# Optimization experiments

Hardware: AMD Instinct MI355X
Metric: run time of the kernel (lower is better)

Reference implementation:

```python
import jax, jax.numpy as jnp
import numpy as np
from jax import lax

NX = NY = NZ = 64
H = 1.0
BIG = 1000.0  # 'infinity' init value used by the torch module
N_EVENT = 4096


def _seed_u0(v, x, y, z):
    """Faithful port of Eikonal3D.set_u0: seed travel time at the 8 grid nodes
    surrounding the source (x,y,z in physical coords), rest = BIG."""
    ix0 = jnp.clip(jnp.floor(x / H), 0, NX - 2).astype(jnp.int32)
    iy0 = jnp.clip(jnp.floor(y / H), 0, NY - 2).astype(jnp.int32)
    iz0 = jnp.clip(jnp.floor(z / H), 0, NZ - 2).astype(jnp.int32)
    xs = jnp.clip(x, 0.0, (NX - 1) * H) / H
    ys = jnp.clip(y, 0.0, (NY - 1) * H) / H
    zs = jnp.clip(z, 0.0, (NZ - 1) * H) / H
    u0 = jnp.full((NX, NY, NZ), BIG, dtype=v.dtype)
    for dx in (0, 1):
        for dy in (0, 1):
            for dz in (0, 1):
                ii, jj, kk = ix0 + dx, iy0 + dy, iz0 + dz
                dist = jnp.sqrt((xs - ii) ** 2 + (ys - jj) ** 2 + (zs - kk) ** 2)
                u0 = u0.at[ii, jj, kk].set(dist * H / v[ii, jj, kk])
    return u0


def _godunov_update(u, fh):
    """One Jacobi pass of the Godunov upwind local eikonal solver |grad u| = f."""
    up = jnp.pad(u, 1, constant_values=BIG * 10.0)
    ax = jnp.minimum(up[:-2, 1:-1, 1:-1], up[2:, 1:-1, 1:-1])
    ay = jnp.minimum(up[1:-1, :-2, 1:-1], up[1:-1, 2:, 1:-1])
    az = jnp.minimum(up[1:-1, 1:-1, :-2], up[1:-1, 1:-1, 2:])
    a = jnp.sort(jnp.stack([ax, ay, az], axis=0), axis=0)
    a1, a2, a3 = a[0], a[1], a[2]
    # 1-direction candidate
    x1 = a1 + fh
    # 2-direction candidate
    d2 = 2.0 * fh * fh - (a1 - a2) ** 2
    x2 = 0.5 * (a1 + a2 + jnp.sqrt(jnp.maximum(d2, 0.0)))
    # 3-direction candidate
    s = a1 + a2 + a3
    q = a1 * a1 + a2 * a2 + a3 * a3
    d3 = s * s - 3.0 * (q - fh * fh)
    x3 = (s + jnp.sqrt(jnp.maximum(d3, 0.0))) / 3.0
    unew = jnp.where(x1 <= a2, x1, jnp.where(x2 <= a3, x2, x3))
    return jnp.minimum(u, unew)


def _interp(tbl, x, y, z):
    """Faithful port of Eikonal3D.interp (trilinear, with the module's exact
    clamp semantics: indices from unclamped coords, weights from clamped)."""
    ix0 = jnp.clip(jnp.floor(x / H), 0, NX - 2).astype(jnp.int32)
    iy0 = jnp.clip(jnp.floor(y / H), 0, NY - 2).astype(jnp.int32)
    iz0 = jnp.clip(jnp.floor(z / H), 0, NZ - 2).astype(jnp.int32)
    ix1, iy1, iz1 = ix0 + 1, iy0 + 1, iz0 + 1
    xs = jnp.clip(x, 0.0, (NX - 1) * H) / H
    ys = jnp.clip(y, 0.0, (NY - 1) * H) / H
    zs = jnp.clip(z, 0.0, (NZ - 1) * H) / H
    wx1, wx0 = ix1 - xs, xs - ix0
    wy1, wy0 = iy1 - ys, ys - iy0
    wz1, wz0 = iz1 - zs, zs - iz0
    t = (tbl[ix0, iy0, iz0] * wx1 * wy1 * wz1 + tbl[ix1, iy0, iz0] * wx0 * wy1 * wz1
         + tbl[ix0, iy1, iz0] * wx1 * wy0 * wz1 + tbl[ix1, iy1, iz0] * wx0 * wy0 * wz1
         + tbl[ix0, iy0, iz1] * wx1 * wy1 * wz0 + tbl[ix1, iy0, iz1] * wx0 * wy1 * wz0
         + tbl[ix0, iy1, iz1] * wx1 * wy0 * wz0 + tbl[ix1, iy1, iz1] * wx0 * wy0 * wz0)
    return t


def setup_inputs() -> dict:
    key = jax.random.key(0)
    k1, k2, k3, k4, k5 = jax.random.split(key, 5)
    vp = 5.0 + 2.0 * jax.random.uniform(k1, (NX, NY, NZ), dtype=jnp.float32)
    station_loc = jax.random.uniform(k2, (3,), dtype=jnp.float32) * (NX - 1) * H
    event_loc = jax.random.uniform(k3, (N_EVENT, 3), dtype=jnp.float32) * (NX - 1) * H
    event_time = jax.random.normal(k4, (N_EVENT,), dtype=jnp.float32)
    phase_time = jax.random.normal(k5, (N_EVENT,), dtype=jnp.float32) + 10.0
    return {"vp": vp, "station_loc": station_loc, "event_loc": event_loc,
            "event_time": event_time, "phase_time": phase_time, "n_iter": 128}


def reference(vp, station_loc, event_loc, event_time, phase_time, n_iter):
    fh = (1.0 / vp) * H  # slowness * grid spacing
    u0 = _seed_u0(vp, station_loc[0], station_loc[1], station_loc[2])
    u, _ = lax.scan(lambda u, _: (_godunov_update(u, fh), None), u0, None, length=n_iter)
    tt = _interp(u, event_loc[:, 0], event_loc[:, 1], event_loc[:, 2])
    at = event_time + tt  # predicted arrival time per pick
    loss = jnp.mean((at - phase_time) ** 2)
    return at, loss
```

## Files before the change

### kernel.cpp

```cpp
#include <hip/hip_runtime.h>
#include <hip/hip_bf16.h>


#define NXg 64
#define NYg 64
#define NZg 64
#define NPTS (NXg * NYg * NZg)
#define BIGV 1000.0f
#define PADV 10000.0f
#define NEV 4096

__global__ __launch_bounds__(256) void eik_init(const float* __restrict__ vp,
                                                const float* __restrict__ st,
                                                float* __restrict__ u,
                                                float* __restrict__ fh) {
    int idx = blockIdx.x * blockDim.x + threadIdx.x;
    if (idx >= NPTS) return;
    float v = vp[idx];
    fh[idx] = 1.0f / v;

    int z = idx & 63;
    int y = (idx >> 6) & 63;
    int x = idx >> 12;

    float sx = st[0], sy = st[1], sz = st[2];
    int ix0 = min(max((int)floorf(sx), 0), NXg - 2);
    int iy0 = min(max((int)floorf(sy), 0), NYg - 2);
    int iz0 = min(max((int)floorf(sz), 0), NZg - 2);
    float xs = fminf(fmaxf(sx, 0.0f), (float)(NXg - 1));
    float ys = fminf(fmaxf(sy, 0.0f), (float)(NYg - 1));
    float zs = fminf(fmaxf(sz, 0.0f), (float)(NZg - 1));

    float val = BIGV;
    if (x >= ix0 && x <= ix0 + 1 && y >= iy0 && y <= iy0 + 1 &&
        z >= iz0 && z <= iz0 + 1) {
        float dx = xs - (float)x;
        float dy = ys - (float)y;
        float dz = zs - (float)z;
        float dist = sqrtf(dx * dx + dy * dy + dz * dz);
        val = dist / v;
    }
    u[idx] = val;
}

__global__ __launch_bounds__(256) void eik_godunov(const float* __restrict__ u,
                                                   float* __restrict__ un,
                                                   const float* __restrict__ fh) {
    int idx = blockIdx.x * blockDim.x + threadIdx.x;
    if (idx >= NPTS) return;
    int z = idx & 63;
    int y = (idx >> 6) & 63;
    int x = idx >> 12;

    float uc = u[idx];
    float xm = (x > 0)       ? u[idx - 4096] : PADV;
    float xp = (x < NXg - 1) ? u[idx + 4096] : PADV;
    float ym = (y > 0)       ? u[idx - 64]   : PADV;
    float yp = (y < NYg - 1) ? u[idx + 64]   : PADV;
    float zm = (z > 0)       ? u[idx - 1]    : PADV;
    float zp = (z < NZg - 1) ? u[idx + 1]    : PADV;

    float ax = fminf(xm, xp);
    float ay = fminf(ym, yp);
    float az = fminf(zm, zp);

    float lo = fminf(ax, ay), hi = fmaxf(ax, ay);
    float a1 = fminf(lo, az);
    float a3 = fmaxf(hi, az);
    float a2 = fminf(fmaxf(lo, az), hi);

    float f = fh[idx];

    float x1 = a1 + f;
    float d12 = a1 - a2;
    float d2 = 2.0f * f * f - d12 * d12;
    float x2 = 0.5f * (a1 + a2 + sqrtf(fmaxf(d2, 0.0f)));
    float s = a1 + a2 + a3;
    float q = a1 * a1 + a2 * a2 + a3 * a3;
    float d3 = s * s - 3.0f * (q - f * f);
    float x3 = (s + sqrtf(fmaxf(d3, 0.0f))) * (1.0f / 3.0f);

    float unew = (x1 <= a2) ? x1 : ((x2 <= a3) ? x2 : x3);
    un[idx] = fminf(uc, unew);
}

__global__ __launch_bounds__(1024) void eik_finalize(const float* __restrict__ u,
                                                     const float* __restrict__ evloc,
                                                     const float* __restrict__ evtime,
                                                     const float* __restrict__ phtime,
                                                     float* __restrict__ out) {
    __shared__ float red[16];
    int t = threadIdx.x;
    float acc = 0.0f;
    for (int i = t; i < NEV; i += 1024) {
        float x = evloc[3 * i + 0];
        float y = evloc[3 * i + 1];
        float z = evloc[3 * i + 2];
        int ix0 = min(max((int)floorf(x), 0), NXg - 2);
        int iy0 = min(max((int)floorf(y), 0), NYg - 2);
        int iz0 = min(max((int)floorf(z), 0), NZg - 2);
        float xs = fminf(fmaxf(x, 0.0f), (float)(NXg - 1));
        float ys = fminf(fmaxf(y, 0.0f), (float)(NYg - 1));
        float zs = fminf(fmaxf(z, 0.0f), (float)(NZg - 1));
        float wx0 = xs - (float)ix0, wx1 = (float)(ix0 + 1) - xs;
        float wy0 = ys - (float)iy0, wy1 = (float)(iy0 + 1) - ys;
        float wz0 = zs - (float)iz0, wz1 = (float)(iz0 + 1) - zs;
        int base = ix0 * 4096 + iy0 * 64 + iz0;
        float c000 = u[base];
        float c100 = u[base + 4096];
        float c010 = u[base + 64];
        float c110 = u[base + 4096 + 64];
        float c001 = u[base + 1];
        float c101 = u[base + 4096 + 1];
        float c011 = u[base + 64 + 1];
        float c111 = u[base + 4096 + 64 + 1];
        float tt = c000 * wx1 * wy1 * wz1 + c100 * wx0 * wy1 * wz1
                 + c010 * wx1 * wy0 * wz1 + c110 * wx0 * wy0 * wz1
                 + c001 * wx1 * wy1 * wz0 + c101 * wx0 * wy1 * wz0
                 + c011 * wx1 * wy0 * wz0 + c111 * wx0 * wy0 * wz0;
        float at = evtime[i] + tt;
        out[i] = at;
        float d = at - phtime[i];
        acc += d * d;
    }
    #pragma unroll
    for (int off = 32; off > 0; off >>= 1) acc += __shfl_down(acc, off);
    if ((t & 63) == 0) red[t >> 6] = acc;
    __syncthreads();
    if (t < 16) {
        float v = red[t];
        #pragma unroll
        for (int off = 8; off > 0; off >>= 1) v += __shfl_down(v, off);
        if (t == 0) out[NEV] = v * (1.0f / (float)NEV);
    }
}

extern "C" void kernel_launch(void* const* d_in, const int* in_sizes, int n_in,
                              void* d_out, int out_size, void* d_ws, size_t ws_size,
                              hipStream_t stream) {
    const float* vp     = (const float*)d_in[0];
    const float* stloc  = (const float*)d_in[1];
    const float* evloc  = (const float*)d_in[2];
    const float* evtime = (const float*)d_in[3];
    const float* phtime = (const float*)d_in[4];
    float* out = (float*)d_out;

    float* w   = (float*)d_ws;
    float* u0  = w;
    float* u1  = w + NPTS;
    float* fh  = w + 2 * NPTS;

    const int NITER = 128;

    eik_init<<<NPTS / 256, 256, 0, stream>>>(vp, stloc, u0, fh);

    float* cur = u0;
    float* nxt = u1;
    for (int it = 0; it < NITER; ++it) {
        eik_godunov<<<NPTS / 256, 256, 0, stream>>>(cur, nxt, fh);
        float* tmp = cur; cur = nxt; nxt = tmp;
    }

    eik_finalize<<<1, 1024, 0, stream>>>(cur, evloc, evtime, phtime, out);
}
```

Before: 355.5 us.

## Fuse four Jacobi sweeps per launch with halo tiles and skip converged blocks

Replaces the 128 per-sweep launches with 32 launches. Each launch loads an 8^3 tile plus a 4-cell halo into LDS and runs four Godunov sweeps on shrinking regions, which removes most launches and global memory traffic. It also keeps per-block change flags. A block whose 27 neighbours did not change in the previous group just copies its tile forward. This adds redundant halo compute, higher LDS use, and flag bookkeeping that must stay exact with respect to the Jacobi semantics.

```diff
diff --git a/kernel.cpp b/kernel.cpp
--- a/kernel.cpp
+++ b/kernel.cpp
@@ -3,74 +3,24 @@
 
 
 #define NXg 64
-#define NYg 64
-#define NZg 64
-#define NPTS (NXg * NYg * NZg)
+#define NPTS (64 * 64 * 64)
 #define BIGV 1000.0f
 #define PADV 10000.0f
 #define NEV 4096
 
-__global__ __launch_bounds__(256) void eik_init(const float* __restrict__ vp,
-                                                const float* __restrict__ st,
-                                                float* __restrict__ u,
-                                                float* __restrict__ fh) {
-    int idx = blockIdx.x * blockDim.x + threadIdx.x;
-    if (idx >= NPTS) return;
-    float v = vp[idx];
-    fh[idx] = 1.0f / v;
-
-    int z = idx & 63;
-    int y = (idx >> 6) & 63;
-    int x = idx >> 12;
-
-    float sx = st[0], sy = st[1], sz = st[2];
-    int ix0 = min(max((int)floorf(sx), 0), NXg - 2);
-    int iy0 = min(max((int)floorf(sy), 0), NYg - 2);
-    int iz0 = min(max((int)floorf(sz), 0), NZg - 2);
-    float xs = fminf(fmaxf(sx, 0.0f), (float)(NXg - 1));
-    float ys = fminf(fmaxf(sy, 0.0f), (float)(NYg - 1));
-    float zs = fminf(fmaxf(sz, 0.0f), (float)(NZg - 1));
-
-    float val = BIGV;
-    if (x >= ix0 && x <= ix0 + 1 && y >= iy0 && y <= iy0 + 1 &&
-        z >= iz0 && z <= iz0 + 1) {
-        float dx = xs - (float)x;
-        float dy = ys - (float)y;
-        float dz = zs - (float)z;
-        float dist = sqrtf(dx * dx + dy * dy + dz * dz);
-        val = dist / v;
-    }
-    u[idx] = val;
-}
-
-__global__ __launch_bounds__(256) void eik_godunov(const float* __restrict__ u,
-                                                   float* __restrict__ un,
-                                                   const float* __restrict__ fh) {
-    int idx = blockIdx.x * blockDim.x + threadIdx.x;
-    if (idx >= NPTS) return;
-    int z = idx & 63;
-    int y = (idx >> 6) & 63;
-    int x = idx >> 12;
-
-    float uc = u[idx];
-    float xm = (x > 0)       ? u[idx - 4096] : PADV;
-    float xp = (x < NXg - 1) ? u[idx + 4096] : PADV;
-    float ym = (y > 0)       ? u[idx - 64]   : PADV;
-    float yp = (y < NYg - 1) ? u[idx + 64]   : PADV;
-    float zm = (z > 0)       ? u[idx - 1]    : PADV;
-    float zp = (z < NZg - 1) ? u[idx + 1]    : PADV;
-
-    float ax = fminf(xm, xp);
-    float ay = fminf(ym, yp);
-    float az = fminf(zm, zp);
-
+#define TB 8
+#define HALO 4
+#define RB 16
+#define ZS 20
+#define NBLK 512
+#define NGROUPS 32
+
+__device__ __forceinline__ float godunov_cell(float uc, float ax, float ay,
+                                              float az, float f) {
     float lo = fminf(ax, ay), hi = fmaxf(ax, ay);
     float a1 = fminf(lo, az);
     float a3 = fmaxf(hi, az);
     float a2 = fminf(fmaxf(lo, az), hi);
-
-    float f = fh[idx];
-
     float x1 = a1 + f;
     float d12 = a1 - a2;
     float d2 = 2.0f * f * f - d12 * d12;
@@ -79,9 +29,178 @@
     float q = a1 * a1 + a2 * a2 + a3 * a3;
     float d3 = s * s - 3.0f * (q - f * f);
     float x3 = (s + sqrtf(fmaxf(d3, 0.0f))) * (1.0f / 3.0f);
-
     float unew = (x1 <= a2) ? x1 : ((x2 <= a3) ? x2 : x3);
-    un[idx] = fminf(uc, unew);
+    return fminf(uc, unew);
+}
+
+__global__ __launch_bounds__(256) void eik_init(const float* __restrict__ vp,
+                                                const float* __restrict__ st,
+                                                float* __restrict__ u,
+                                                float* __restrict__ fh,
+                                                int* __restrict__ flags0) {
+    int idx = blockIdx.x * blockDim.x + threadIdx.x;
+    if (idx >= NPTS) return;
+    float v = vp[idx];
+    fh[idx] = 1.0f / v;
+
+    if (idx < NBLK) flags0[idx] = 1;
+
+    int z = idx & 63;
+    int y = (idx >> 6) & 63;
+    int x = idx >> 12;
+
+    float sx = st[0], sy = st[1], sz = st[2];
+    int ix0 = min(max((int)floorf(sx), 0), 62);
+    int iy0 = min(max((int)floorf(sy), 0), 62);
+    int iz0 = min(max((int)floorf(sz), 0), 62);
+    float xs = fminf(fmaxf(sx, 0.0f), 63.0f);
+    float ys = fminf(fmaxf(sy, 0.0f), 63.0f);
+    float zs = fminf(fmaxf(sz, 0.0f), 63.0f);
+
+    float val = BIGV;
+    if (x >= ix0 && x <= ix0 + 1 && y >= iy0 && y <= iy0 + 1 &&
+        z >= iz0 && z <= iz0 + 1) {
+        float dx = xs - (float)x;
+        float dy = ys - (float)y;
+        float dz = zs - (float)z;
+        val = sqrtf(dx * dx + dy * dy + dz * dz) / v;
+    }
+    u[idx] = val;
+}
+
+__global__ __launch_bounds__(256, 3) void eik_group(
+    const float* __restrict__ uCur, float* __restrict__ uNext,
+    const float* __restrict__ fh,
+    const int* __restrict__ chPrev, int* __restrict__ chNext) {
+    __shared__ float A[RB * RB * ZS];
+    __shared__ float B[RB * RB * ZS];
+    __shared__ float stash[TB * TB * TB];
+    __shared__ int s_any;
+
+    const int b = blockIdx.x;
+    const int BX = b >> 6, BY = (b >> 3) & 7, BZ = b & 7;
+    const int ox = BX * TB - HALO, oy = BY * TB - HALO, oz = BZ * TB - HALO;
+    const int tid = threadIdx.x;
+    const int tbase = ((BX * TB) * 64 + BY * TB) * 64 + BZ * TB;
+
+    if (tid == 0) s_any = 0;
+    __syncthreads();
+    if (tid < 27) {
+        int dx = tid / 9 - 1, dy = (tid / 3) % 3 - 1, dz = tid % 3 - 1;
+        int nx = BX + dx, ny = BY + dy, nz = BZ + dz;
+        if (nx >= 0 && nx < 8 && ny >= 0 && ny < 8 && nz >= 0 && nz < 8) {
+            if (chPrev[(nx << 6) | (ny << 3) | nz]) atomicOr(&s_any, 1);
+        }
+    }
+    __syncthreads();
+
+    if (!s_any) {
+        for (int u = tid; u < TB * TB * 2; u += 256) {
+            int c = u & 1, r = u >> 1;
+            int lx = r >> 3, ly = r & 7;
+            int goff = tbase + (lx * 64 + ly) * 64 + 4 * c;
+            *(float4*)&uNext[goff] = *(const float4*)&uCur[goff];
+        }
+        if (tid == 0) chNext[b] = 0;
+        return;
+    }
+
+    for (int u = tid; u < RB * RB * 4; u += 256) {
+        int c = u & 3, r = u >> 2;
+        int lx = r >> 4, ly = r & 15;
+        int gx = ox + lx, gy = oy + ly, gz0 = oz + 4 * c;
+        int loff = (lx * RB + ly) * ZS + 4 * c;
+        float4 v;
+        bool xyok = (gx >= 0) & (gx < 64) & (gy >= 0) & (gy < 64);
+        if (xyok && gz0 >= 0 && gz0 + 3 < 64) {
+            v = *(const float4*)&uCur[(gx * 64 + gy) * 64 + gz0];
+        } else {
+            int gb = (gx * 64 + gy) * 64;
+            v.x = (xyok && gz0 + 0 >= 0 && gz0 + 0 < 64) ? uCur[gb + gz0 + 0] : PADV;
+            v.y = (xyok && gz0 + 1 >= 0 && gz0 + 1 < 64) ? uCur[gb + gz0 + 1] : PADV;
+            v.z = (xyok && gz0 + 2 >= 0 && gz0 + 2 < 64) ? uCur[gb + gz0 + 2] : PADV;
+            v.w = (xyok && gz0 + 3 >= 0 && gz0 + 3 < 64) ? uCur[gb + gz0 + 3] : PADV;
+        }
+        *(float4*)&A[loff] = v;
+        *(float4*)&B[loff] = v;
+    }
+    __syncthreads();
+
+    for (int u = tid; u < TB * TB * 2; u += 256) {
+        int c = u & 1, r = u >> 1;
+        int lx = r >> 3, ly = r & 7;
+        int loff = ((lx + 4) * RB + (ly + 4)) * ZS + 4 + 4 * c;
+        *(float4*)&stash[(lx * 8 + ly) * 8 + 4 * c] = *(const float4*)&A[loff];
+    }
+
+    #pragma unroll
+    for (int it = 0; it < HALO; ++it) {
+        __syncthreads();
+        const float* src = (it & 1) ? B : A;
+        float* dst = (it & 1) ? A : B;
+        const int s0 = it + 1, s1 = 14 - it;
+        const int S = s1 - s0 + 1;
+        const int units = S * S * 4;
+        const int lzlo = max(s0, -oz);
+        const int lzhi = min(s1, 63 - oz);
+        for (int u = tid; u < units; u += 256) {
+            int c = u & 3, r = u >> 2;
+            int ly = s0 + (r % S), lx = s0 + (r / S);
+            int zb = 4 * c;
+            int rowoff = (lx * RB + ly) * ZS;
+            float4 cc = *(const float4*)&src[rowoff + zb];
+            float zmm = src[rowoff + zb - 1];
+            float zpp = src[rowoff + zb + 4];
+            float4 xm = *(const float4*)&src[rowoff - RB * ZS + zb];
+            float4 xp = *(const float4*)&src[rowoff + RB * ZS + zb];
+            float4 ym = *(const float4*)&src[rowoff - ZS + zb];
+            float4 yp = *(const float4*)&src[rowoff + ZS + zb];
+
+            int gx = ox + lx, gy = oy + ly, gz0 = oz + zb;
+            int cgx = min(max(gx, 0), 63), cgy = min(max(gy, 0), 63);
+            int cgz = min(max(gz0, 0), 60);
+            float4 f4 = *(const float4*)&fh[(cgx * 64 + cgy) * 64 + cgz];
+
+            float o0 = godunov_cell(cc.x, fminf(xm.x, xp.x), fminf(ym.x, yp.x),
+                                    fminf(zmm, cc.y), f4.x);
+            float o1 = godunov_cell(cc.y, fminf(xm.y, xp.y), fminf(ym.y, yp.y),
+                                    fminf(cc.x, cc.z), f4.y);
+            float o2 = godunov_cell(cc.z, fminf(xm.z, xp.z), fminf(ym.z, yp.z),
+                                    fminf(cc.y, cc.w), f4.z);
+            float o3 = godunov_cell(cc.w, fminf(xm.w, xp.w), fminf(ym.w, yp.w),
+                                    fminf(cc.z, zpp), f4.w);
+
+            bool xyin = (gx >= 0) & (gx < 64) & (gy >= 0) & (gy < 64);
+            int jlo = max(lzlo - zb, 0), jhi = min(lzhi - zb, 3);
+            if (xyin & (jlo == 0) & (jhi == 3)) {
+                *(float4*)&dst[rowoff + zb] = make_float4(o0, o1, o2, o3);
+            } else if (xyin) {
+                if (jlo <= 0 && 0 <= jhi) dst[rowoff + zb + 0] = o0;
+                if (jlo <= 1 && 1 <= jhi) dst[rowoff + zb + 1] = o1;
+                if (jlo <= 2 && 2 <= jhi) dst[rowoff + zb + 2] = o2;
+                if (jlo <= 3 && 3 <= jhi) dst[rowoff + zb + 3] = o3;
+            }
+        }
+    }
+    __syncthreads();
+
+    if (tid == 0) s_any = 0;
+    __syncthreads();
+    int changed = 0;
+    for (int u = tid; u < TB * TB * 2; u += 256) {
+        int c = u & 1, r = u >> 1;
+        int lx = r >> 3, ly = r & 7;
+        int loff = ((lx + 4) * RB + (ly + 4)) * ZS + 4 + 4 * c;
+        float4 v = *(const float4*)&A[loff];
+        float4 sv = *(const float4*)&stash[(lx * 8 + ly) * 8 + 4 * c];
+        int goff = tbase + (lx * 64 + ly) * 64 + 4 * c;
+        *(float4*)&uNext[goff] = v;
+        if (v.x != sv.x || v.y != sv.y || v.z != sv.z || v.w != sv.w) changed = 1;
+    }
+    int wch = __any(changed);
+    if ((tid & 63) == 0 && wch) atomicOr(&s_any, 1);
+    __syncthreads();
+    if (tid == 0) chNext[b] = s_any;
 }
 
 __global__ __launch_bounds__(1024) void eik_finalize(const float* __restrict__ u,
@@ -96,12 +215,12 @@
         float x = evloc[3 * i + 0];
         float y = evloc[3 * i + 1];
         float z = evloc[3 * i + 2];
-        int ix0 = min(max((int)floorf(x), 0), NXg - 2);
-        int iy0 = min(max((int)floorf(y), 0), NYg - 2);
-        int iz0 = min(max((int)floorf(z), 0), NZg - 2);
-        float xs = fminf(fmaxf(x, 0.0f), (float)(NXg - 1));
-        float ys = fminf(fmaxf(y, 0.0f), (float)(NYg - 1));
-        float zs = fminf(fmaxf(z, 0.0f), (float)(NZg - 1));
+        int ix0 = min(max((int)floorf(x), 0), 62);
+        int iy0 = min(max((int)floorf(y), 0), 62);
+        int iz0 = min(max((int)floorf(z), 0), 62);
+        float xs = fminf(fmaxf(x, 0.0f), 63.0f);
+        float ys = fminf(fmaxf(y, 0.0f), 63.0f);
+        float zs = fminf(fmaxf(z, 0.0f), 63.0f);
         float wx0 = xs - (float)ix0, wx1 = (float)(ix0 + 1) - xs;
         float wy0 = ys - (float)iy0, wy1 = (float)(iy0 + 1) - ys;
         float wz0 = zs - (float)iz0, wz1 = (float)(iz0 + 1) - zs;
@@ -145,21 +264,22 @@
     const float* phtime = (const float*)d_in[4];
     float* out = (float*)d_out;
 
-    float* w   = (float*)d_ws;
-    float* u0  = w;
-    float* u1  = w + NPTS;
-    float* fh  = w + 2 * NPTS;
-
-    const int NITER = 128;
-
-    eik_init<<<NPTS / 256, 256, 0, stream>>>(vp, stloc, u0, fh);
-
-    float* cur = u0;
-    float* nxt = u1;
-    for (int it = 0; it < NITER; ++it) {
-        eik_godunov<<<NPTS / 256, 256, 0, stream>>>(cur, nxt, fh);
-        float* tmp = cur; cur = nxt; nxt = tmp;
-    }
-
-    eik_finalize<<<1, 1024, 0, stream>>>(cur, evloc, evtime, phtime, out);
-}
+    float* w  = (float*)d_ws;
+    float* uA = w;
+    float* uB = w + NPTS;
+    float* fh = w + 2 * NPTS;
+    int* flA  = (int*)(w + 3 * NPTS);
+    int* flB  = flA + NBLK;
+
+    eik_init<<<NPTS / 256, 256, 0, stream>>>(vp, stloc, uA, fh, flA);
+
+    for (int g = 0; g < NGROUPS; ++g) {
+        const float* s = (g & 1) ? uB : uA;
+        float*       d = (g & 1) ? uA : uB;
+        const int*  fp = (g & 1) ? flB : flA;
+        int*        fn = (g & 1) ? flA : flB;
+        eik_group<<<NBLK, 256, 0, stream>>>(s, d, fh, fp, fn);
+    }
+
+    eik_finalize<<<1, 1024, 0, stream>>>(uA, evloc, evtime, phtime, out);
+}
```

New measurement: 574.2 us. 61.5% more time.

## Fuse four Jacobi sweeps per launch with halo tiles and skip converged blocks

Applied to the files above, without the earlier changes.

Replaces 128 single-sweep launches with 32 launches. Each launch runs four Jacobi iterations on an 8x8x8 block tile with a 4-cell halo held in registers and shared memory. Each block also records whether its values changed, and a block is skipped (plain copy) when it and its 26 neighbours were unchanged in the previous group. This cuts launch overhead and global-memory traffic in exchange for redundant halo compute. Skipping blocks relies on the fixed point being exact, and any mismatch in the halo or flag logic could cause divergence from the reference.

```diff
diff --git a/kernel.cpp b/kernel.cpp
--- a/kernel.cpp
+++ b/kernel.cpp
@@ -2,75 +2,19 @@
 #include <hip/hip_bf16.h>
 
 
-#define NXg 64
-#define NYg 64
-#define NZg 64
-#define NPTS (NXg * NYg * NZg)
+#define NPTS (64 * 64 * 64)
 #define BIGV 1000.0f
 #define PADV 10000.0f
 #define NEV 4096
-
-__global__ __launch_bounds__(256) void eik_init(const float* __restrict__ vp,
-                                                const float* __restrict__ st,
-                                                float* __restrict__ u,
-                                                float* __restrict__ fh) {
-    int idx = blockIdx.x * blockDim.x + threadIdx.x;
-    if (idx >= NPTS) return;
-    float v = vp[idx];
-    fh[idx] = 1.0f / v;
-
-    int z = idx & 63;
-    int y = (idx >> 6) & 63;
-    int x = idx >> 12;
-
-    float sx = st[0], sy = st[1], sz = st[2];
-    int ix0 = min(max((int)floorf(sx), 0), NXg - 2);
-    int iy0 = min(max((int)floorf(sy), 0), NYg - 2);
-    int iz0 = min(max((int)floorf(sz), 0), NZg - 2);
-    float xs = fminf(fmaxf(sx, 0.0f), (float)(NXg - 1));
-    float ys = fminf(fmaxf(sy, 0.0f), (float)(NYg - 1));
-    float zs = fminf(fmaxf(sz, 0.0f), (float)(NZg - 1));
-
-    float val = BIGV;
-    if (x >= ix0 && x <= ix0 + 1 && y >= iy0 && y <= iy0 + 1 &&
-        z >= iz0 && z <= iz0 + 1) {
-        float dx = xs - (float)x;
-        float dy = ys - (float)y;
-        float dz = zs - (float)z;
-        float dist = sqrtf(dx * dx + dy * dy + dz * dz);
-        val = dist / v;
-    }
-    u[idx] = val;
-}
-
-__global__ __launch_bounds__(256) void eik_godunov(const float* __restrict__ u,
-                                                   float* __restrict__ un,
-                                                   const float* __restrict__ fh) {
-    int idx = blockIdx.x * blockDim.x + threadIdx.x;
-    if (idx >= NPTS) return;
-    int z = idx & 63;
-    int y = (idx >> 6) & 63;
-    int x = idx >> 12;
-
-    float uc = u[idx];
-    float xm = (x > 0)       ? u[idx - 4096] : PADV;
-    float xp = (x < NXg - 1) ? u[idx + 4096] : PADV;
-    float ym = (y > 0)       ? u[idx - 64]   : PADV;
-    float yp = (y < NYg - 1) ? u[idx + 64]   : PADV;
-    float zm = (z > 0)       ? u[idx - 1]    : PADV;
-    float zp = (z < NZg - 1) ? u[idx + 1]    : PADV;
-
-    float ax = fminf(xm, xp);
-    float ay = fminf(ym, yp);
-    float az = fminf(zm, zp);
-
+#define NBLK 512
+#define NPH 32
+
+__device__ __forceinline__ float godunov_cell(float uc, float ax, float ay,
+                                              float az, float f) {
     float lo = fminf(ax, ay), hi = fmaxf(ax, ay);
     float a1 = fminf(lo, az);
     float a3 = fmaxf(hi, az);
     float a2 = fminf(fmaxf(lo, az), hi);
-
-    float f = fh[idx];
-
     float x1 = a1 + f;
     float d12 = a1 - a2;
     float d2 = 2.0f * f * f - d12 * d12;
@@ -79,9 +23,152 @@
     float q = a1 * a1 + a2 * a2 + a3 * a3;
     float d3 = s * s - 3.0f * (q - f * f);
     float x3 = (s + sqrtf(fmaxf(d3, 0.0f))) * (1.0f / 3.0f);
-
     float unew = (x1 <= a2) ? x1 : ((x2 <= a3) ? x2 : x3);
-    un[idx] = fminf(uc, unew);
+    return fminf(uc, unew);
+}
+
+__device__ __forceinline__ float4 upd_chunk(float4 cc, float4 xm, float4 xp,
+                                            float4 ym, float4 yp,
+                                            float zprev, float znext, float4 f,
+                                            int zb, int zlo, int zhi) {
+    float n0 = godunov_cell(cc.x, fminf(xm.x, xp.x), fminf(ym.x, yp.x), fminf(zprev, cc.y), f.x);
+    float n1 = godunov_cell(cc.y, fminf(xm.y, xp.y), fminf(ym.y, yp.y), fminf(cc.x, cc.z), f.y);
+    float n2 = godunov_cell(cc.z, fminf(xm.z, xp.z), fminf(ym.z, yp.z), fminf(cc.y, cc.w), f.z);
+    float n3 = godunov_cell(cc.w, fminf(xm.w, xp.w), fminf(ym.w, yp.w), fminf(cc.z, znext), f.w);
+    float4 r;
+    r.x = (zb + 0 >= zlo && zb + 0 <= zhi) ? n0 : cc.x;
+    r.y = (zb + 1 >= zlo && zb + 1 <= zhi) ? n1 : cc.y;
+    r.z = (zb + 2 >= zlo && zb + 2 <= zhi) ? n2 : cc.z;
+    r.w = (zb + 3 >= zlo && zb + 3 <= zhi) ? n3 : cc.w;
+    return r;
+}
+
+__global__ __launch_bounds__(256) void eik_init(const float* __restrict__ vp,
+                                                const float* __restrict__ st,
+                                                float* __restrict__ u,
+                                                float* __restrict__ fh,
+                                                int* __restrict__ flA) {
+    int idx = blockIdx.x * blockDim.x + threadIdx.x;
+    if (idx >= NPTS) return;
+    float v = vp[idx];
+    fh[idx] = 1.0f / v;
+
+    if (idx < NBLK) flA[idx] = 1;
+
+    int z = idx & 63;
+    int y = (idx >> 6) & 63;
+    int x = idx >> 12;
+
+    float sx = st[0], sy = st[1], sz = st[2];
+    int ix0 = min(max((int)floorf(sx), 0), 62);
+    int iy0 = min(max((int)floorf(sy), 0), 62);
+    int iz0 = min(max((int)floorf(sz), 0), 62);
+    float xs = fminf(fmaxf(sx, 0.0f), 63.0f);
+    float ys = fminf(fmaxf(sy, 0.0f), 63.0f);
+    float zs = fminf(fmaxf(sz, 0.0f), 63.0f);
+
+    float val = BIGV;
+    if (x >= ix0 && x <= ix0 + 1 && y >= iy0 && y <= iy0 + 1 &&
+        z >= iz0 && z <= iz0 + 1) {
+        float dx = xs - (float)x;
+        float dy = ys - (float)y;
+        float dz = zs - (float)z;
+        val = sqrtf(dx * dx + dy * dy + dz * dz) / v;
+    }
+    u[idx] = val;
+}
+
+__global__ __launch_bounds__(256) void eik_group(
+    const float* __restrict__ src, float* __restrict__ dst,
+    const float* __restrict__ fh,
+    const int* __restrict__ fp, int* __restrict__ fn) {
+    __shared__ float4 cols[4 * 256];
+    __shared__ int s_any;
+
+    const int b = blockIdx.x;
+    const int BX = b >> 6, BY = (b >> 3) & 7, BZ = b & 7;
+    const int t = threadIdx.x;
+    const int lx = t >> 4, ly = t & 15;
+    const int gx = BX * 8 - 4 + lx, gy = BY * 8 - 4 + ly;
+    const int oz = BZ * 8 - 4;
+    const bool xyin = (gx >= 0) & (gx < 64) & (gy >= 0) & (gy < 64);
+    const int rowbase = (xyin ? (gx * 64 + gy) * 64 : 0);
+    const int moz = -oz, mzt = 63 - oz;
+    const bool zin0 = (oz >= 0), zin3 = (oz + 12 <= 60);
+    const bool writer = (lx >= 4) & (lx <= 11) & (ly >= 4) & (ly <= 11);
+
+    if (t == 0) s_any = 0;
+    __syncthreads();
+    if (t < 27) {
+        int dx = t / 9 - 1, dy = (t / 3) % 3 - 1, dz = t % 3 - 1;
+        int nx = BX + dx, ny = BY + dy, nz = BZ + dz;
+        if (nx >= 0 && nx < 8 && ny >= 0 && ny < 8 && nz >= 0 && nz < 8)
+            if (fp[(nx << 6) | (ny << 3) | nz]) atomicOr(&s_any, 1);
+    }
+    __syncthreads();
+    const int active = s_any;
+    __syncthreads();
+
+    if (!active) {
+        if (writer) {
+            *(float4*)&dst[rowbase + oz + 4] = *(const float4*)&src[rowbase + oz + 4];
+            *(float4*)&dst[rowbase + oz + 8] = *(const float4*)&src[rowbase + oz + 8];
+        }
+        if (t == 0) fn[b] = 0;
+        return;
+    }
+
+    const int cgx = min(max(gx, 0), 63), cgy = min(max(gy, 0), 63);
+    const int fb = (cgx * 64 + cgy) * 64;
+    const float4 f0 = *(const float4*)&fh[fb + max(oz, 0)];
+    const float4 f1 = *(const float4*)&fh[fb + oz + 4];
+    const float4 f2 = *(const float4*)&fh[fb + oz + 8];
+    const float4 f3 = *(const float4*)&fh[fb + min(oz + 12, 60)];
+    const float4 PAD4 = make_float4(PADV, PADV, PADV, PADV);
+
+    float4 cc0 = (xyin && zin0) ? *(const float4*)&src[rowbase + oz]      : PAD4;
+    float4 cc1 = xyin           ? *(const float4*)&src[rowbase + oz + 4]  : PAD4;
+    float4 cc2 = xyin           ? *(const float4*)&src[rowbase + oz + 8]  : PAD4;
+    float4 cc3 = (xyin && zin3) ? *(const float4*)&src[rowbase + oz + 12] : PAD4;
+    const float4 st1 = cc1, st2 = cc2;
+
+    #pragma unroll
+    for (int it = 0; it < 4; ++it) {
+        cols[t] = cc0; cols[256 + t] = cc1;
+        cols[512 + t] = cc2; cols[768 + t] = cc3;
+        __syncthreads();
+        const int s0 = it + 1, s1 = 14 - it;
+        if ((lx >= s0) & (lx <= s1) & (ly >= s0) & (ly <= s1) & xyin) {
+            const int zlo = max(s0, moz), zhi = min(s1, mzt);
+            float4 xm0 = cols[t - 16], xp0 = cols[t + 16];
+            float4 ym0 = cols[t - 1],  yp0 = cols[t + 1];
+            float4 xm1 = cols[256 + t - 16], xp1 = cols[256 + t + 16];
+            float4 ym1 = cols[256 + t - 1],  yp1 = cols[256 + t + 1];
+            float4 xm2 = cols[512 + t - 16], xp2 = cols[512 + t + 16];
+            float4 ym2 = cols[512 + t - 1],  yp2 = cols[512 + t + 1];
+            float4 xm3 = cols[768 + t - 16], xp3 = cols[768 + t + 16];
+            float4 ym3 = cols[768 + t - 1],  yp3 = cols[768 + t + 1];
+            float4 n0 = upd_chunk(cc0, xm0, xp0, ym0, yp0, cc0.x, cc1.x, f0, 0,  zlo, zhi);
+            float4 n1 = upd_chunk(cc1, xm1, xp1, ym1, yp1, cc0.w, cc2.x, f1, 4,  zlo, zhi);
+            float4 n2 = upd_chunk(cc2, xm2, xp2, ym2, yp2, cc1.w, cc3.x, f2, 8,  zlo, zhi);
+            float4 n3 = upd_chunk(cc3, xm3, xp3, ym3, yp3, cc2.w, cc3.w, f3, 12, zlo, zhi);
+            cc0 = n0; cc1 = n1; cc2 = n2; cc3 = n3;
+        }
+        __syncthreads();
+    }
+
+    if (t == 0) s_any = 0;
+    __syncthreads();
+    int chg = 0;
+    if (writer) {
+        *(float4*)&dst[rowbase + oz + 4] = cc1;
+        *(float4*)&dst[rowbase + oz + 8] = cc2;
+        chg = (cc1.x != st1.x) | (cc1.y != st1.y) | (cc1.z != st1.z) | (cc1.w != st1.w) |
+              (cc2.x != st2.x) | (cc2.y != st2.y) | (cc2.z != st2.z) | (cc2.w != st2.w);
+    }
+    if (__any(chg) && (t & 63) == 0) atomicOr(&s_any, 1);
+    __syncthreads();
+    if (t == 0) fn[b] = s_any;
 }
 
 __global__ __launch_bounds__(1024) void eik_finalize(const float* __restrict__ u,
@@ -96,28 +183,20 @@
         float x = evloc[3 * i + 0];
         float y = evloc[3 * i + 1];
         float z = evloc[3 * i + 2];
-        int ix0 = min(max((int)floorf(x), 0), NXg - 2);
-        int iy0 = min(max((int)floorf(y), 0), NYg - 2);
-        int iz0 = min(max((int)floorf(z), 0), NZg - 2);
-        float xs = fminf(fmaxf(x, 0.0f), (float)(NXg - 1));
-        float ys = fminf(fmaxf(y, 0.0f), (float)(NYg - 1));
-        float zs = fminf(fmaxf(z, 0.0f), (float)(NZg - 1));
+        int ix0 = min(max((int)floorf(x), 0), 62);
+        int iy0 = min(max((int)floorf(y), 0), 62);
+        int iz0 = min(max((int)floorf(z), 0), 62);
+        float xs = fminf(fmaxf(x, 0.0f), 63.0f);
+        float ys = fminf(fmaxf(y, 0.0f), 63.0f);
+        float zs = fminf(fmaxf(z, 0.0f), 63.0f);
         float wx0 = xs - (float)ix0, wx1 = (float)(ix0 + 1) - xs;
         float wy0 = ys - (float)iy0, wy1 = (float)(iy0 + 1) - ys;
         float wz0 = zs - (float)iz0, wz1 = (float)(iz0 + 1) - zs;
         int base = ix0 * 4096 + iy0 * 64 + iz0;
-        float c000 = u[base];
-        float c100 = u[base + 4096];
-        float c010 = u[base + 64];
-        float c110 = u[base + 4096 + 64];
-        float c001 = u[base + 1];
-        float c101 = u[base + 4096 + 1];
-        float c011 = u[base + 64 + 1];
-        float c111 = u[base + 4096 + 64 + 1];
-        float tt = c000 * wx1 * wy1 * wz1 + c100 * wx0 * wy1 * wz1
-                 + c010 * wx1 * wy0 * wz1 + c110 * wx0 * wy0 * wz1
-                 + c001 * wx1 * wy1 * wz0 + c101 * wx0 * wy1 * wz0
-                 + c011 * wx1 * wy0 * wz0 + c111 * wx0 * wy0 * wz0;
+        float tt = u[base]             * wx1 * wy1 * wz1 + u[base + 4096]          * wx0 * wy1 * wz1
+                 + u[base + 64]        * wx1 * wy0 * wz1 + u[base + 4096 + 64]     * wx0 * wy0 * wz1
+                 + u[base + 1]         * wx1 * wy1 * wz0 + u[base + 4096 + 1]      * wx0 * wy1 * wz0
+                 + u[base + 64 + 1]    * wx1 * wy0 * wz0 + u[base + 4096 + 64 + 1] * wx0 * wy0 * wz0;
         float at = evtime[i] + tt;
         out[i] = at;
         float d = at - phtime[i];
@@ -145,21 +224,22 @@
     const float* phtime = (const float*)d_in[4];
     float* out = (float*)d_out;
 
-    float* w   = (float*)d_ws;
-    float* u0  = w;
-    float* u1  = w + NPTS;
-    float* fh  = w + 2 * NPTS;
-
-    const int NITER = 128;
-
-    eik_init<<<NPTS / 256, 256, 0, stream>>>(vp, stloc, u0, fh);
-
-    float* cur = u0;
-    float* nxt = u1;
-    for (int it = 0; it < NITER; ++it) {
-        eik_godunov<<<NPTS / 256, 256, 0, stream>>>(cur, nxt, fh);
-        float* tmp = cur; cur = nxt; nxt = tmp;
-    }
-
-    eik_finalize<<<1, 1024, 0, stream>>>(cur, evloc, evtime, phtime, out);
-}
+    float* w  = (float*)d_ws;
+    float* uA = w;
+    float* uB = w + NPTS;
+    float* fh = w + 2 * NPTS;
+    int* flA  = (int*)(w + 3 * NPTS);
+    int* flB  = flA + NBLK;
+
+    eik_init<<<NPTS / 256, 256, 0, stream>>>(vp, stloc, uA, fh, flA);
+
+    for (int g = 0; g < NPH; ++g) {
+        const float* s = (g & 1) ? uB : uA;
+        float*       d = (g & 1) ? uA : uB;
+        const int*  fp = (g & 1) ? flB : flA;
+        int*        fn = (g & 1) ? flA : flB;
+        eik_group<<<NBLK, 256, 0, stream>>>(s, d, fh, fp, fn);
+    }
+
+    eik_finalize<<<1, 1024, 0, stream>>>(uA, evloc, evtime, phtime, out);
+}
```

Measured after the change: 582.5 us. 1.64x slower.
